# Kernel tuning notes

Hardware: AMD Instinct MI355X
Metric: run time of the kernel (lower is better)

Reference implementation:

```python
import jax, jax.numpy as jnp
import numpy as np

G, N, C, H, L = 128, 512, 64, 4, 4   # graphs, nodes/graph, channels, heads, layers
NT = G * N                            # 65536 total nodes
PE, IN_DIM, PROT = 16, 64, 128
DEG = 16
E = NT * DEG
EPS = 1e-5


def setup_inputs() -> dict:
    key = jax.random.key(0)
    ks = jax.random.split(key, 48)
    def w(k, shape):
        fan = shape[-2] if len(shape) >= 2 else shape[-1]
        return (jax.random.normal(k, shape, jnp.float32) / np.sqrt(fan)).astype(jnp.float32)
    inp = {}
    inp['x'] = jax.random.normal(ks[0], (NT, IN_DIM), jnp.float32)
    inp['pe'] = jax.random.normal(ks[1], (NT, PE), jnp.float32)
    inp['edge_index'] = jax.random.randint(ks[2], (2, E), 0, NT, dtype=jnp.int32)
    # embedding layers
    inp['node_emb_w'] = w(ks[3], (IN_DIM, C - PE)); inp['node_emb_b'] = jnp.zeros((C - PE,), jnp.float32)
    inp['pe_lin_w'] = w(ks[4], (PE, PE));           inp['pe_lin_b'] = jnp.zeros((PE,), jnp.float32)
    inp['pe_norm_g'] = jnp.ones((PE,), jnp.float32); inp['pe_norm_b'] = jnp.zeros((PE,), jnp.float32)
    # per-layer stacked params [L, ...]
    inp['gin_w1'] = w(ks[5], (L, C, C)); inp['gin_b1'] = jnp.zeros((L, C), jnp.float32)
    inp['gin_w2'] = w(ks[6], (L, C, C)); inp['gin_b2'] = jnp.zeros((L, C), jnp.float32)
    inp['attn_wq'] = w(ks[7], (L, C, C)); inp['attn_bq'] = jnp.zeros((L, C), jnp.float32)
    inp['attn_wk'] = w(ks[8], (L, C, C)); inp['attn_bk'] = jnp.zeros((L, C), jnp.float32)
    inp['attn_wv'] = w(ks[9], (L, C, C)); inp['attn_bv'] = jnp.zeros((L, C), jnp.float32)
    inp['attn_wo'] = w(ks[10], (L, C, C)); inp['attn_bo'] = jnp.zeros((L, C), jnp.float32)
    for i, nm in enumerate(['norm1', 'norm2', 'norm3']):
        inp[nm + '_g'] = jnp.ones((L, C), jnp.float32)
        inp[nm + '_b'] = jnp.zeros((L, C), jnp.float32)
    inp['mlp_w1'] = w(ks[11], (L, C, 2 * C)); inp['mlp_b1'] = jnp.zeros((L, 2 * C), jnp.float32)
    inp['mlp_w2'] = w(ks[12], (L, 2 * C, C)); inp['mlp_b2'] = jnp.zeros((L, C), jnp.float32)
    inp['head_w'] = w(ks[13], (C, PROT)); inp['head_b'] = jnp.zeros((PROT,), jnp.float32)
    return inp


def _bn(x, g, b):
    # BatchNorm1d, training-mode batch statistics (biased variance)
    mu = x.mean(axis=0)
    var = jnp.mean((x - mu) ** 2, axis=0)
    return (x - mu) * jax.lax.rsqrt(var + EPS) * g + b


def _mha(xd, wq, bq, wk, bk, wv, bv, wo, bo):
    # xd: [G, N, C] dense per-graph batch (all graphs equal size -> full mask)
    dh = C // H
    q = (xd @ wq + bq).reshape(G, N, H, dh)
    k = (xd @ wk + bk).reshape(G, N, H, dh)
    v = (xd @ wv + bv).reshape(G, N, H, dh)
    s = jnp.einsum('gqhd,gkhd->ghqk', q, k) * (1.0 / np.sqrt(dh))
    a = jax.nn.softmax(s, axis=-1)
    o = jnp.einsum('ghqk,gkhd->gqhd', a, v).reshape(G, N, C)
    return o @ wo + bo


def reference(x, pe, edge_index, node_emb_w, node_emb_b, pe_lin_w, pe_lin_b,
              pe_norm_g, pe_norm_b, gin_w1, gin_b1, gin_w2, gin_b2,
              attn_wq, attn_bq, attn_wk, attn_bk, attn_wv, attn_bv, attn_wo, attn_bo,
              norm1_g, norm1_b, norm2_g, norm2_b, norm3_g, norm3_b,
              mlp_w1, mlp_b1, mlp_w2, mlp_b2, head_w, head_b):
    src, dst = edge_index[0], edge_index[1]
    pe_n = _bn(pe, pe_norm_g, pe_norm_b)
    h = jnp.concatenate([x @ node_emb_w + node_emb_b, pe_n @ pe_lin_w + pe_lin_b], axis=1)  # [NT, C]
    for l in range(L):
        # local: GINConv (eps=0): nn(x + sum_j x_j) via gather + segment_sum
        agg = jax.ops.segment_sum(h[src], dst, num_segments=NT)
        z = h + agg
        hl = jax.nn.relu(z @ gin_w1[l] + gin_b1[l]) @ gin_w2[l] + gin_b2[l]
        hl = _bn(hl + h, norm1_g[l], norm1_b[l])
        # global: dense multihead self-attention per graph
        ha = _mha(h.reshape(G, N, C), attn_wq[l], attn_bq[l], attn_wk[l], attn_bk[l],
                  attn_wv[l], attn_bv[l], attn_wo[l], attn_bo[l]).reshape(NT, C)
        ha = _bn(ha + h, norm2_g[l], norm2_b[l])
        out = hl + ha
        out = out + (jax.nn.relu(out @ mlp_w1[l] + mlp_b1[l]) @ mlp_w2[l] + mlp_b2[l])
        h = _bn(out, norm3_g[l], norm3_b[l])
    pooled = h.reshape(G, N, C).mean(axis=1)  # global_mean_pool over equal-size graphs
    return pooled @ head_w + head_b
```

## Files before the change

### kernel.cpp

```cpp
#include <hip/hip_runtime.h>

typedef unsigned short ushort;
typedef unsigned int uint;
typedef __attribute__((ext_vector_type(8))) short short8;
typedef __attribute__((ext_vector_type(4))) float floatx4;

#define NTOT   65536
#define CH     64
#define NLAYER 4
#define NEDGE  1048576
#define EPSV   1e-5f

#define OW_EMB 0
#define OB_EMB 3072
#define OW_PE  3120
#define OB_PE  3376
#define OG_PEN 3392
#define OB_PEN 3408
#define OW_G1  3424
#define OB_G1  19808
#define OW_G2  20064
#define OB_G2  36448
#define OW_Q   36704
#define OB_Q   53088
#define OW_K   53344
#define OB_K   69728
#define OW_V   69984
#define OB_V   86368
#define OW_O   86624
#define OB_O   103008
#define ON1G   103264
#define ON1B   103520
#define ON2G   103776
#define ON2B   104032
#define ON3G   104288
#define ON3B   104544
#define OW_M1  104800
#define OB_M1  137568
#define OW_M2  138080
#define OB_M2  170848
#define OW_H   171104
#define OB_H   179296
#define TOTW   179424

__device__ __forceinline__ float bf2f(ushort u){ return __uint_as_float(((uint)u) << 16); }
__device__ __forceinline__ ushort f2bf(float f){
    uint u = __float_as_uint(f);
    uint r = (u + 0x7fffu + ((u >> 16) & 1u)) >> 16;
    return (ushort)r;
}
__device__ __forceinline__ float2 bfp2(uint w){
    return make_float2(__uint_as_float(w << 16), __uint_as_float(w & 0xffff0000u));
}
__device__ __forceinline__ short8 ldf(const ushort* p){ return *(const short8*)p; }
__device__ __forceinline__ floatx4 mfma16(short8 a, short8 b, floatx4 c){
    return __builtin_amdgcn_mfma_f32_16x16x32_bf16(a, b, c, 0, 0, 0);
}
__device__ __forceinline__ void bnfin(float* sf, const float* st, const ushort* g,
                                      const ushort* b, int ident, int t){
    if (t < 64){
        float a, bb;
        if (ident){ a = 1.f; bb = 0.f; }
        else {
            float mu  = st[t] * (1.f / NTOT);
            float var = st[64 + t] * (1.f / NTOT) - mu * mu;
            a = rsqrtf(var + EPSV) * bf2f(g[t]);
            bb = bf2f(b[t]) - mu * a;
        }
        sf[t] = a; sf[64 + t] = bb;
    }
}

__global__ void detect_k(const uint* __restrict__ x, int* __restrict__ flag){
    int lane = threadIdx.x;
    uint w = x[lane];
    uint e = (w >> 7) & 0xffu;
    int ok = (e >= 100u && e <= 140u) ? 1 : 0;
    unsigned long long m = __ballot(ok);
    if (lane == 0) flag[0] = (__popcll(m) >= 48) ? 1 : 0;
}

struct WPtrs { const void* p[30]; };

__global__ void convall_k(WPtrs ptrs, ushort* __restrict__ dst, const int* __restrict__ flag){
    const int offs[31] = {0,3072,3120,3376,3392,3408,3424,19808,20064,36448,36704,
                          53088,53344,69728,69984,86368,86624,103008,103264,103520,
                          103776,104032,104288,104544,104800,137568,138080,170848,
                          171104,179296,179424};
    const int kdt[30] = {64,0,16,0,0,0, 64,0,64,0, 64,0,64,0,64,0,64,0,
                         0,0,0,0,0,0, 64,0,128,0, 64,0};
    const int ndt[30] = {48,0,16,0,0,0, 64,0,64,0, 64,0,64,0,64,0,64,0,
                         0,0,0,0,0,0, 128,0,64,0, 128,0};
    int i = blockIdx.x * blockDim.x + threadIdx.x;
    if (i >= TOTW) return;
    int s = 0;
    while (s < 29 && i >= offs[s + 1]) ++s;
    int j = i - offs[s];
    int srcj = j;
    int K = kdt[s];
    if (K > 0){
        int N = ndt[s], KN = K * N;
        int l = j / KN, r = j - l * KN;
        int n = r / K, k2 = r - n * K;
        srcj = l * KN + k2 * N + n;
    }
    if (*flag) dst[i] = ((const ushort*)ptrs.p[s])[srcj];
    else       dst[i] = f2bf(((const float*)ptrs.p[s])[srcj]);
}

__global__ void pe_stats_k(const void* __restrict__ peraw, const int* __restrict__ flag,
                           float* __restrict__ stats){
    int bf = *flag;
    int t = threadIdx.x;
    int c = t & 15, rb = t >> 4;
    int row0 = blockIdx.x * 256;
    float s = 0.f, ss = 0.f;
    for (int i = 0; i < 16; ++i){
        int r = row0 + rb + 16 * i;
        size_t idx = (size_t)r * 16 + c;
        float v = bf ? bf2f(((const ushort*)peraw)[idx]) : ((const float*)peraw)[idx];
        s += v; ss += v * v;
    }
    __shared__ float red[256];
    red[t] = s; __syncthreads();
    if (t < 16){ float tot = 0.f; for (int j = 0; j < 16; ++j) tot += red[t + 16 * j]; atomicAdd(&stats[t], tot); }
    __syncthreads();
    red[t] = ss; __syncthreads();
    if (t < 16){ float tot = 0.f; for (int j = 0; j < 16; ++j) tot += red[t + 16 * j]; atomicAdd(&stats[64 + t], tot); }
}

__global__ void fin_k(const float* __restrict__ stats, const ushort* __restrict__ g,
                      const ushort* __restrict__ b, float* __restrict__ fin, int nch){
    int c = threadIdx.x;
    if (c >= nch) return;
    float mu  = stats[c] * (1.f / NTOT);
    float var = stats[64 + c] * (1.f / NTOT) - mu * mu;
    float a = rsqrtf(var + EPSV) * bf2f(g[c]);
    fin[c] = a;
    fin[64 + c] = bf2f(b[c]) - mu * a;
}

__global__ void embed_k(const void* __restrict__ xraw, const void* __restrict__ peraw,
                        const int* __restrict__ flag, const ushort* __restrict__ wsa,
                        const float* __restrict__ finpe, ushort* __restrict__ hout){
    __shared__ __align__(16) ushort xb[64 * 72];
    __shared__ __align__(16) ushort pen[64 * 24];
    __shared__ __align__(16) ushort Wes[48 * 72];
    __shared__ __align__(16) ushort Wps[16 * 24];
    int bf = *flag;
    int t = threadIdx.x;
    int row0 = blockIdx.x * 64;
    if (bf){
        const uint* xsrc = (const uint*)((const ushort*)xraw + (size_t)row0 * 64);
        for (int i = t; i < 2048; i += 256){
            int r = i >> 5, u = i & 31;
            ((uint*)(xb + r * 72))[u] = xsrc[i];
        }
    } else {
        const float4* xsrc = (const float4*)((const float*)xraw + (size_t)row0 * 64);
        for (int i = t; i < 1024; i += 256){
            int r = i >> 4, u = i & 15;
            float4 f = xsrc[i];
            ((uint*)(xb + r * 72))[2 * u]     = (uint)f2bf(f.x) | ((uint)f2bf(f.y) << 16);
            ((uint*)(xb + r * 72))[2 * u + 1] = (uint)f2bf(f.z) | ((uint)f2bf(f.w) << 16);
        }
    }
    for (int i = t; i < 1024; i += 256){
        int r = i >> 4, k = i & 15;
        size_t idx = (size_t)(row0 + r) * 16 + k;
        float v = bf ? bf2f(((const ushort*)peraw)[idx]) : ((const float*)peraw)[idx];
        pen[r * 24 + k] = f2bf(v * finpe[k] + finpe[64 + k]);
    }
    for (int i = t; i < 1536; i += 256){
        int r = i >> 5, u = i & 31;
        ((uint*)(Wes + r * 72))[u] = ((const uint*)(wsa + OW_EMB))[i];
    }
    {
        int r = t >> 4, k = t & 15;
        Wps[r * 24 + k] = wsa[OW_PE + t];
    }
    __syncthreads();
    int w = t >> 6, l = t & 63, m = l & 15, quad = l >> 4;
    const short8 zero8 = {0, 0, 0, 0, 0, 0, 0, 0};
    const floatx4 zf4 = {0.f, 0.f, 0.f, 0.f};
    const ushort* ap = xb + (16 * w + m) * 72 + quad * 8;
    short8 a0 = ldf(ap), a1 = ldf(ap + 32);
    short8 ape = (quad < 2) ? ldf(pen + (16 * w + m) * 24 + quad * 8) : zero8;
    #pragma unroll
    for (int nt = 0; nt < 4; ++nt){
        floatx4 c = zf4;
        float bias;
        if (nt < 3){
            const ushort* bp = Wes + (nt * 16 + m) * 72 + quad * 8;
            c = mfma16(a0, ldf(bp), c);
            c = mfma16(a1, ldf(bp + 32), c);
            bias = bf2f(wsa[OB_EMB + nt * 16 + m]);
        } else {
            short8 bpe = (quad < 2) ? ldf(Wps + m * 24 + quad * 8) : zero8;
            c = mfma16(ape, bpe, c);
            bias = bf2f(wsa[OB_PE + m]);
        }
        #pragma unroll
        for (int r = 0; r < 4; ++r)
            hout[(size_t)(row0 + 16 * w + quad * 4 + r) * 64 + nt * 16 + m] = f2bf(c[r] + bias);
    }
}

__global__ void hist_k(const int* __restrict__ dst, int* __restrict__ cnt){
    int stride = gridDim.x * blockDim.x;
    for (int e = blockIdx.x * blockDim.x + threadIdx.x; e < NEDGE; e += stride)
        atomicAdd(&cnt[dst[e]], 1);
}

__global__ void scan_k(const int* __restrict__ cnt, int* __restrict__ offs, int* __restrict__ cur){
    int t = threadIdx.x;
    int base0 = t * 64;
    int s = 0;
    for (int i = 0; i < 64; ++i) s += cnt[base0 + i];
    __shared__ int pref[1024];
    pref[t] = s; __syncthreads();
    for (int off = 1; off < 1024; off <<= 1){
        int v = (t >= off) ? pref[t - off] : 0;
        __syncthreads();
        pref[t] += v;
        __syncthreads();
    }
    int run = pref[t] - s;
    for (int i = 0; i < 64; ++i){
        offs[base0 + i] = run;
        cur[base0 + i]  = run;
        run += cnt[base0 + i];
    }
    if (t == 1023) offs[65536] = run;
}

__global__ void scatter_k(const int* __restrict__ src, const int* __restrict__ dst,
                          int* __restrict__ cur, int* __restrict__ csr){
    int stride = gridDim.x * blockDim.x;
    for (int e = blockIdx.x * blockDim.x + threadIdx.x; e < NEDGE; e += stride){
        int p = atomicAdd(&cur[dst[e]], 1);
        atomicExch(&csr[p], src[e]);
    }
}

__global__ void agg_k(const ushort* __restrict__ h, const int* __restrict__ offs,
                      const int* __restrict__ csr, ushort* __restrict__ z,
                      const float* __restrict__ st, const ushort* __restrict__ g,
                      const ushort* __restrict__ b, int ident){
    __shared__ float sf[128];
    int t = threadIdx.x;
    bnfin(sf, st, g, b, ident, t);
    __syncthreads();
    int w = t >> 6, l = t & 63;
    int node = blockIdx.x * 8 + w * 2 + (l >> 5);
    int c2 = l & 31;
    const uint* hp = (const uint*)h;
    int beg = offs[node], end = offs[node + 1];
    float2 s = bfp2(hp[(size_t)node * 32 + c2]);
    for (int i = beg; i < end; ++i){
        int sn = csr[i];
        float2 p = bfp2(hp[(size_t)sn * 32 + c2]);
        s.x += p.x; s.y += p.y;
    }
    float n = (float)(1 + end - beg);
    int c0 = c2 * 2;
    float o0 = sf[c0] * s.x + n * sf[64 + c0];
    float o1 = sf[c0 + 1] * s.y + n * sf[64 + c0 + 1];
    ((uint*)z)[(size_t)node * 32 + c2] = (uint)f2bf(o0) | ((uint)f2bf(o1) << 16);
}

__global__ void ginqkv_k(const ushort* __restrict__ z, const ushort* __restrict__ h,
                         const float* __restrict__ st3, const ushort* __restrict__ g3,
                         const ushort* __restrict__ b3, int ident,
                         const ushort* __restrict__ W1, const ushort* __restrict__ b1,
                         const ushort* __restrict__ W2, const ushort* __restrict__ b2,
                         const ushort* __restrict__ Wq, const ushort* __restrict__ bq,
                         const ushort* __restrict__ Wk, const ushort* __restrict__ bk,
                         const ushort* __restrict__ Wv, const ushort* __restrict__ bv,
                         ushort* __restrict__ zout, ushort* __restrict__ qo,
                         ushort* __restrict__ ko, ushort* __restrict__ vo,
                         float* __restrict__ stats){
    __shared__ __align__(16) ushort As[64 * 72];
    __shared__ __align__(16) ushort Hs[64 * 72];
    __shared__ __align__(16) ushort W1s[64 * 72];
    __shared__ __align__(16) ushort W2s[64 * 72];
    __shared__ __align__(16) ushort Wqs[64 * 72];
    __shared__ __align__(16) ushort Wks[64 * 72];
    __shared__ __align__(16) ushort Wvs[64 * 72];
    __shared__ float sb[128];
    __shared__ float sf[128];
    int t = threadIdx.x;
    int row0 = blockIdx.x * 64;
    bnfin(sf, st3, g3, b3, ident, t);
    if (t < 128) sb[t] = 0.f;
    __syncthreads();
    for (int i = t; i < 2048; i += 256){
        int r = i >> 5, u = i & 31;
        ((uint*)(As  + r * 72))[u] = ((const uint*)(z + (size_t)row0 * 64))[i];
        uint hv = ((const uint*)(h + (size_t)row0 * 64))[i];
        int c0 = u * 2;
        float2 p = bfp2(hv);
        ((uint*)(Hs + r * 72))[u] = (uint)f2bf(p.x * sf[c0] + sf[64 + c0])
                                  | ((uint)f2bf(p.y * sf[c0 + 1] + sf[64 + c0 + 1]) << 16);
        ((uint*)(W1s + r * 72))[u] = ((const uint*)W1)[i];
        ((uint*)(W2s + r * 72))[u] = ((const uint*)W2)[i];
        ((uint*)(Wqs + r * 72))[u] = ((const uint*)Wq)[i];
        ((uint*)(Wks + r * 72))[u] = ((const uint*)Wk)[i];
        ((uint*)(Wvs + r * 72))[u] = ((const uint*)Wv)[i];
    }
    __syncthreads();
    int w = t >> 6, l = t & 63, m = l & 15, q4 = l >> 4;
    const ushort* ap = As + (16 * w + m) * 72 + q4 * 8;
    short8 a0 = ldf(ap), a1 = ldf(ap + 32);
    const ushort* hpp = Hs + (16 * w + m) * 72 + q4 * 8;
    short8 h0 = ldf(hpp), h1 = ldf(hpp + 32);
    floatx4 acc[4];
    #pragma unroll
    for (int nt = 0; nt < 4; ++nt){
        const ushort* bp = W1s + (nt * 16 + m) * 72 + q4 * 8;
        floatx4 c = {0.f, 0.f, 0.f, 0.f};
        c = mfma16(a0, ldf(bp), c);
        c = mfma16(a1, ldf(bp + 32), c);
        acc[nt] = c;
    }
    #pragma unroll
    for (int nt = 0; nt < 4; ++nt){
        float bv = bf2f(b1[nt * 16 + m]);
        #pragma unroll
        for (int r = 0; r < 4; ++r)
            As[(16 * w + q4 * 4 + r) * 72 + nt * 16 + m] = f2bf(fmaxf(acc[nt][r] + bv, 0.f));
    }
    const ushort* ap2 = As + (16 * w + m) * 72 + q4 * 8;
    short8 t0 = ldf(ap2), t1 = ldf(ap2 + 32);
    #pragma unroll
    for (int nt = 0; nt < 4; ++nt){
        const ushort* bp = W2s + (nt * 16 + m) * 72 + q4 * 8;
        floatx4 c = {0.f, 0.f, 0.f, 0.f};
        c = mfma16(t0, ldf(bp), c);
        c = mfma16(t1, ldf(bp + 32), c);
        float bv = bf2f(b2[nt * 16 + m]);
        float vs = 0.f, vss = 0.f;
        #pragma unroll
        for (int r = 0; r < 4; ++r){
            int lr = 16 * w + q4 * 4 + r;
            float val = c[r] + bv + bf2f(Hs[lr * 72 + nt * 16 + m]);
            zout[(size_t)(row0 + lr) * 64 + nt * 16 + m] = f2bf(val);
            vs += val; vss += val * val;
        }
        vs  += __shfl_xor(vs, 16, 64);  vs  += __shfl_xor(vs, 32, 64);
        vss += __shfl_xor(vss, 16, 64); vss += __shfl_xor(vss, 32, 64);
        if (q4 == 0){
            atomicAdd(&sb[nt * 16 + m], vs);
            atomicAdd(&sb[64 + nt * 16 + m], vss);
        }
    }
    ushort* outs[3] = {qo, ko, vo};
    const ushort* bias[3] = {bq, bk, bv};
    const ushort* wmats[3] = {Wqs, Wks, Wvs};
    #pragma unroll
    for (int o = 0; o < 3; ++o){
        #pragma unroll
        for (int nt = 0; nt < 4; ++nt){
            const ushort* bp = wmats[o] + (nt * 16 + m) * 72 + q4 * 8;
            floatx4 c = {0.f, 0.f, 0.f, 0.f};
            c = mfma16(h0, ldf(bp), c);
            c = mfma16(h1, ldf(bp + 32), c);
            float bv2 = bf2f(bias[o][nt * 16 + m]);
            #pragma unroll
            for (int r = 0; r < 4; ++r)
                outs[o][(size_t)(row0 + 16 * w + q4 * 4 + r) * 64 + nt * 16 + m] = f2bf(c[r] + bv2);
        }
    }
    __syncthreads();
    if (t < 64){
        atomicAdd(&stats[t], sb[t]);
        atomicAdd(&stats[64 + t], sb[64 + t]);
    }
}

__global__ void attn_k(ushort* __restrict__ q, const ushort* __restrict__ k,
                       const ushort* __restrict__ v){
    __shared__ __align__(16) ushort Ks[512 * 24];
    __shared__ __align__(16) ushort Vt[16 * 536];
    int t = threadIdx.x;
    int g = blockIdx.x >> 2, head = blockIdx.x & 3;
    int base = g * 512;
    for (int i = t; i < 4096; i += 256){
        int n = i >> 3, u = i & 7;
        uint kw = ((const uint*)(k + (size_t)(base + n) * 64 + head * 16))[u];
        uint vw = ((const uint*)(v + (size_t)(base + n) * 64 + head * 16))[u];
        float2 kf = bfp2(kw);
        Ks[n * 24 + 2 * u]     = f2bf(kf.x * 0.25f);
        Ks[n * 24 + 2 * u + 1] = f2bf(kf.y * 0.25f);
        Vt[(2 * u) * 536 + n]     = (ushort)(vw & 0xffffu);
        Vt[(2 * u + 1) * 536 + n] = (ushort)(vw >> 16);
    }
    __syncthreads();
    int w = t >> 6, l = t & 63, m16 = l & 15, quad = l >> 4;
    const short8 zero8 = {0, 0, 0, 0, 0, 0, 0, 0};
    const floatx4 zf4 = {0.f, 0.f, 0.f, 0.f};
    int key1 = ((m16 >> 2) << 3) + (m16 & 3);

    for (int qi = 0; qi < 8; ++qi){
        int qt = w * 8 + qi;
        int qrow = base + qt * 16 + m16;
        short8 qf = zero8;
        if (quad < 2) qf = ldf(q + (size_t)qrow * 64 + head * 16 + quad * 8);
        floatx4 O = zf4;
        float mm = -1e30f, ll = 0.f;
        for (int kg = 0; kg < 16; ++kg){
            int kb = kg * 32;
            short8 af1 = zero8, af2 = zero8;
            if (quad < 2){
                const ushort* kp = Ks + (kb + key1) * 24 + quad * 8;
                af1 = ldf(kp);
                af2 = ldf(kp + 96);
            }
            floatx4 s1 = mfma16(af1, qf, zf4);
            floatx4 s2 = mfma16(af2, qf, zf4);
            float tm = fmaxf(fmaxf(fmaxf(s1[0], s1[1]), fmaxf(s1[2], s1[3])),
                             fmaxf(fmaxf(s2[0], s2[1]), fmaxf(s2[2], s2[3])));
            tm = fmaxf(tm, __shfl_xor(tm, 16, 64));
            tm = fmaxf(tm, __shfl_xor(tm, 32, 64));
            float mn = fmaxf(mm, tm);
            float c = __expf(mm - mn);
            float p0 = __expf(s1[0] - mn), p1 = __expf(s1[1] - mn);
            float p2 = __expf(s1[2] - mn), p3 = __expf(s1[3] - mn);
            float p4 = __expf(s2[0] - mn), p5 = __expf(s2[1] - mn);
            float p6 = __expf(s2[2] - mn), p7 = __expf(s2[3] - mn);
            float ts = ((p0 + p1) + (p2 + p3)) + ((p4 + p5) + (p6 + p7));
            ts += __shfl_xor(ts, 16, 64);
            ts += __shfl_xor(ts, 32, 64);
            ll = ll * c + ts;
            mm = mn;
            short8 pf;
            pf[0] = (short)f2bf(p0); pf[1] = (short)f2bf(p1);
            pf[2] = (short)f2bf(p2); pf[3] = (short)f2bf(p3);
            pf[4] = (short)f2bf(p4); pf[5] = (short)f2bf(p5);
            pf[6] = (short)f2bf(p6); pf[7] = (short)f2bf(p7);
            short8 vf = ldf(Vt + m16 * 536 + kb + quad * 8);
            O[0] *= c; O[1] *= c; O[2] *= c; O[3] *= c;
            O = mfma16(vf, pf, O);
        }
        float inv = 1.f / ll;
        uint lo = (uint)f2bf(O[0] * inv) | ((uint)f2bf(O[1] * inv) << 16);
        uint hi = (uint)f2bf(O[2] * inv) | ((uint)f2bf(O[3] * inv) << 16);
        uint2 st = {lo, hi};
        *(uint2*)(q + (size_t)qrow * 64 + head * 16 + quad * 4) = st;
    }
}

__global__ void oproj_k(ushort* __restrict__ o, const ushort* __restrict__ h,
                        const float* __restrict__ st3, const ushort* __restrict__ g3,
                        const ushort* __restrict__ b3, int ident,
                        const ushort* __restrict__ Wo, const ushort* __restrict__ bo,
                        float* __restrict__ stats){
    __shared__ __align__(16) ushort As[64 * 72];
    __shared__ __align__(16) ushort Ws[64 * 72];
    __shared__ float sb[128];
    __shared__ float sf[128];
    int t = threadIdx.x;
    int row0 = blockIdx.x * 64;
    bnfin(sf, st3, g3, b3, ident, t);
    if (t < 128) sb[t] = 0.f;
    __syncthreads();
    for (int i = t; i < 2048; i += 256){
        int r = i >> 5, u = i & 31;
        ((uint*)(As + r * 72))[u] = ((const uint*)(o + (size_t)row0 * 64))[i];
        ((uint*)(Ws + r * 72))[u] = ((const uint*)Wo)[i];
    }
    __syncthreads();
    int w = t >> 6, l = t & 63, m = l & 15, q4 = l >> 4;
    const ushort* ap = As + (16 * w + m) * 72 + q4 * 8;
    short8 a0 = ldf(ap), a1 = ldf(ap + 32);
    #pragma unroll
    for (int nt = 0; nt < 4; ++nt){
        const ushort* bp = Ws + (nt * 16 + m) * 72 + q4 * 8;
        floatx4 c = {0.f, 0.f, 0.f, 0.f};
        c = mfma16(a0, ldf(bp), c);
        c = mfma16(a1, ldf(bp + 32), c);
        int ch = nt * 16 + m;
        float bv = bf2f(bo[ch]);
        float ba = sf[ch], bb = sf[64 + ch];
        float vs = 0.f, vss = 0.f;
        #pragma unroll
        for (int r = 0; r < 4; ++r){
            size_t gi = (size_t)(row0 + 16 * w + q4 * 4 + r) * 64 + ch;
            float val = c[r] + bv + ba * bf2f(h[gi]) + bb;
            o[gi] = f2bf(val);
            vs += val; vss += val * val;
        }
        vs  += __shfl_xor(vs, 16, 64);  vs  += __shfl_xor(vs, 32, 64);
        vss += __shfl_xor(vss, 16, 64); vss += __shfl_xor(vss, 32, 64);
        if (q4 == 0){
            atomicAdd(&sb[ch], vs);
            atomicAdd(&sb[64 + ch], vss);
        }
    }
    __syncthreads();
    if (t < 64){
        atomicAdd(&stats[t], sb[t]);
        atomicAdd(&stats[64 + t], sb[64 + t]);
    }
}

__global__ void comb_k(const ushort* __restrict__ hlpre, const ushort* __restrict__ hapre,
                       const float* __restrict__ st1, const ushort* __restrict__ n1g,
                       const ushort* __restrict__ n1b,
                       const float* __restrict__ st2, const ushort* __restrict__ n2g,
                       const ushort* __restrict__ n2b,
                       const ushort* __restrict__ W1, const ushort* __restrict__ b1,
                       const ushort* __restrict__ W2, const ushort* __restrict__ b2,
                       ushort* __restrict__ hout, float* __restrict__ stats){
    __shared__ __align__(16) ushort Ob[64 * 72];
    __shared__ float Of[64 * 64];
    __shared__ __align__(16) ushort W1s[128 * 72];
    __shared__ __align__(16) ushort Hs[64 * 136];
    __shared__ __align__(16) ushort W2s[64 * 136];
    __shared__ float sb[128];
    __shared__ float sf1[128], sf2[128];
    int t = threadIdx.x;
    int row0 = blockIdx.x * 64;
    if (t < 128){
        const float* st = (t < 64) ? st1 : st2;
        const ushort* g = (t < 64) ? n1g : n2g;
        const ushort* b = (t < 64) ? n1b : n2b;
        float* f = (t < 64) ? sf1 : sf2;
        int c = t & 63;
        float mu  = st[c] * (1.f / NTOT);
        float var = st[64 + c] * (1.f / NTOT) - mu * mu;
        float a = rsqrtf(var + EPSV) * bf2f(g[c]);
        f[c] = a;
        f[64 + c] = bf2f(b[c]) - mu * a;
        sb[t] = 0.f;
    }
    __syncthreads();
    for (int i = t; i < 2048; i += 256){
        int r = i >> 5, u = i & 31;
        size_t gi = (size_t)(row0 + r) * 32 + u;
        uint wl = ((const uint*)hlpre)[gi], wa = ((const uint*)hapre)[gi];
        int c0 = u * 2;
        float2 pl = bfp2(wl), pa = bfp2(wa);
        float v0 = pl.x * sf1[c0] + sf1[64 + c0] + pa.x * sf2[c0] + sf2[64 + c0];
        float v1 = pl.y * sf1[c0 + 1] + sf1[64 + c0 + 1] + pa.y * sf2[c0 + 1] + sf2[64 + c0 + 1];
        ((uint*)(Ob + r * 72))[u] = (uint)f2bf(v0) | ((uint)f2bf(v1) << 16);
        Of[r * 64 + c0] = v0; Of[r * 64 + c0 + 1] = v1;
    }
    for (int i = t; i < 4096; i += 256){
        int r = i >> 5, u = i & 31;
        ((uint*)(W1s + r * 72))[u] = ((const uint*)W1)[i];
        int r2 = i >> 6, u2 = i & 63;
        ((uint*)(W2s + r2 * 136))[u2] = ((const uint*)W2)[i];
    }
    __syncthreads();
    int w = t >> 6, l = t & 63, m = l & 15, q4 = l >> 4;
    const ushort* ap = Ob + (16 * w + m) * 72 + q4 * 8;
    short8 a0 = ldf(ap), a1 = ldf(ap + 32);
    #pragma unroll
    for (int nt = 0; nt < 8; ++nt){
        const ushort* bp = W1s + (nt * 16 + m) * 72 + q4 * 8;
        floatx4 c = {0.f, 0.f, 0.f, 0.f};
        c = mfma16(a0, ldf(bp), c);
        c = mfma16(a1, ldf(bp + 32), c);
        float bv = bf2f(b1[nt * 16 + m]);
        #pragma unroll
        for (int r = 0; r < 4; ++r)
            Hs[(16 * w + q4 * 4 + r) * 136 + nt * 16 + m] = f2bf(fmaxf(c[r] + bv, 0.f));
    }
    const ushort* ap2 = Hs + (16 * w + m) * 136 + q4 * 8;
    short8 h0 = ldf(ap2), h1 = ldf(ap2 + 32), h2 = ldf(ap2 + 64), h3 = ldf(ap2 + 96);
    #pragma unroll
    for (int nt = 0; nt < 4; ++nt){
        const ushort* bp = W2s + (nt * 16 + m) * 136 + q4 * 8;
        floatx4 c = {0.f, 0.f, 0.f, 0.f};
        c = mfma16(h0, ldf(bp), c);
        c = mfma16(h1, ldf(bp + 32), c);
        c = mfma16(h2, ldf(bp + 64), c);
        c = mfma16(h3, ldf(bp + 96), c);
        float bv = bf2f(b2[nt * 16 + m]);
        float vs = 0.f, vss = 0.f;
        #pragma unroll
        for (int r = 0; r < 4; ++r){
            int lr = 16 * w + q4 * 4 + r;
            float val = c[r] + bv + Of[lr * 64 + nt * 16 + m];
            hout[(size_t)(row0 + lr) * 64 + nt * 16 + m] = f2bf(val);
            vs += val; vss += val * val;
        }
        vs  += __shfl_xor(vs, 16, 64);  vs  += __shfl_xor(vs, 32, 64);
        vss += __shfl_xor(vss, 16, 64); vss += __shfl_xor(vss, 32, 64);
        if (q4 == 0){
            atomicAdd(&sb[nt * 16 + m], vs);
            atomicAdd(&sb[64 + nt * 16 + m], vss);
        }
    }
    __syncthreads();
    if (t < 64){
        atomicAdd(&stats[t], sb[t]);
        atomicAdd(&stats[64 + t], sb[64 + t]);
    }
}

__global__ void pool_head_k(const ushort* __restrict__ h, const float* __restrict__ st3,
                            const ushort* __restrict__ g3, const ushort* __restrict__ b3,
                            const ushort* __restrict__ Wh, const ushort* __restrict__ bh,
                            const int* __restrict__ flag, void* __restrict__ out){
    __shared__ float red[256];
    __shared__ float pooled[64];
    __shared__ float sf[128];
    int t = threadIdx.x, g = blockIdx.x;
    bnfin(sf, st3, g3, b3, 0, t);
    int c = t & 63, rb = t >> 6;
    float s = 0.f;
    for (int ii = 0; ii < 128; ++ii){
        int r = rb + 4 * ii;
        s += bf2f(h[(size_t)(g * 512 + r) * 64 + c]);
    }
    red[t] = s; __syncthreads();
    if (t < 64)
        pooled[t] = sf[t] * ((red[t] + red[64 + t] + red[128 + t] + red[192 + t]) * (1.f / 512.f))
                  + sf[64 + t];
    __syncthreads();
    if (t < 128){
        float a = bf2f(bh[t]);
        #pragma unroll
        for (int k = 0; k < 64; ++k) a += pooled[k] * bf2f(Wh[t * 64 + k]);
        if (*flag) ((ushort*)out)[(size_t)g * 128 + t] = f2bf(a);
        else       ((float*)out)[(size_t)g * 128 + t] = a;
    }
}

extern "C" void kernel_launch(void* const* d_in, const int* in_sizes, int n_in,
                              void* d_out, int out_size, void* d_ws, size_t ws_size,
                              hipStream_t stream){
    const void* x  = d_in[0];
    const void* pe = d_in[1];
    const int* eidx = (const int*)d_in[2];

    char* ws = (char*)d_ws;
    const size_t MB = 1024 * 1024;
    const size_t KB = 1024;
    ushort* h_buf = (ushort*)(ws);
    ushort* z_buf = (ushort*)(ws + 8 * MB);
    ushort* q_buf = (ushort*)(ws + 16 * MB);
    ushort* k_buf = (ushort*)(ws + 24 * MB);
    ushort* v_buf = (ushort*)(ws + 32 * MB);
    int* csr   = (int*)(ws + 40 * MB);
    int* offs  = (int*)(ws + 44 * MB);
    int* cnt   = (int*)(ws + 44 * MB + 384 * KB);
    int* cur   = (int*)(ws + 44 * MB + 640 * KB);
    float* stats = (float*)(ws + 44 * MB + 896 * KB);
    float* fin   = (float*)(ws + 44 * MB + 904 * KB);
    int*   flag  = (int*)(ws + 44 * MB + 912 * KB);
    ushort* wsa  = (ushort*)(ws + 45 * MB);

    hipMemsetAsync(stats, 0, 13 * 128 * sizeof(float), stream);
    hipMemsetAsync(cnt, 0, 65536 * sizeof(int), stream);

    detect_k<<<1, 64, 0, stream>>>((const uint*)x, flag);

    WPtrs wp;
    for (int i = 0; i < 30; ++i) wp.p[i] = d_in[3 + i];
    convall_k<<<(TOTW + 255) / 256, 256, 0, stream>>>(wp, wsa, flag);

    pe_stats_k<<<256, 256, 0, stream>>>(pe, flag, stats);
    fin_k<<<1, 64, 0, stream>>>(stats, wsa + OG_PEN, wsa + OB_PEN, fin, 16);
    embed_k<<<1024, 256, 0, stream>>>(x, pe, flag, wsa, fin, h_buf);
    hist_k<<<1024, 256, 0, stream>>>(eidx + NEDGE, cnt);
    scan_k<<<1, 1024, 0, stream>>>(cnt, offs, cur);
    scatter_k<<<1024, 256, 0, stream>>>(eidx, eidx + NEDGE, cur, csr);

    for (int l = 0; l < NLAYER; ++l){
        float* st1 = stats + (1 + 3 * l) * 128;
        float* st2 = stats + (2 + 3 * l) * 128;
        float* st3 = stats + (3 + 3 * l) * 128;
        int ident = (l == 0) ? 1 : 0;
        const float* stp = (l == 0) ? stats : stats + (3 * l) * 128;
        const ushort* gp = wsa + ON3G + (l ? (l - 1) : 0) * 64;
        const ushort* bp = wsa + ON3B + (l ? (l - 1) : 0) * 64;

        agg_k<<<8192, 256, 0, stream>>>(h_buf, offs, csr, z_buf, stp, gp, bp, ident);
        ginqkv_k<<<1024, 256, 0, stream>>>(z_buf, h_buf, stp, gp, bp, ident,
                                           wsa + OW_G1 + l * 4096, wsa + OB_G1 + l * 64,
                                           wsa + OW_G2 + l * 4096, wsa + OB_G2 + l * 64,
                                           wsa + OW_Q + l * 4096, wsa + OB_Q + l * 64,
                                           wsa + OW_K + l * 4096, wsa + OB_K + l * 64,
                                           wsa + OW_V + l * 4096, wsa + OB_V + l * 64,
                                           z_buf, q_buf, k_buf, v_buf, st1);
        attn_k<<<512, 256, 0, stream>>>(q_buf, k_buf, v_buf);
        oproj_k<<<1024, 256, 0, stream>>>(q_buf, h_buf, stp, gp, bp, ident,
                                          wsa + OW_O + l * 4096, wsa + OB_O + l * 64, st2);
        comb_k<<<1024, 256, 0, stream>>>(z_buf, q_buf,
                                         st1, wsa + ON1G + l * 64, wsa + ON1B + l * 64,
                                         st2, wsa + ON2G + l * 64, wsa + ON2B + l * 64,
                                         wsa + OW_M1 + l * 8192, wsa + OB_M1 + l * 128,
                                         wsa + OW_M2 + l * 8192, wsa + OB_M2 + l * 64,
                                         h_buf, st3);
    }
    pool_head_k<<<128, 256, 0, stream>>>(h_buf, stats + 12 * 128,
                                         wsa + ON3G + 3 * 64, wsa + ON3B + 3 * 64,
                                         wsa + OW_H, wsa + OB_H, flag, d_out);
}
```

Measured before the change: 1.249 ms.

## Build CSR with two-pass shared-memory bucket sort and 16-bit indices

Replaces the per-edge global atomicAdd/atomicExch scatter with a two-pass build. Pass A bins edges into 256 destination buckets in LDS and writes them out in coalesced chunks with per-bucket global cursors. Pass B sorts each bucket by local node in LDS and writes a compact ushort CSR. Storing source indices as 16-bit also halves the CSR bytes the aggregation kernel reads in every layer. The risk is that it relies on a 65536-node limit and fixed LDS capacities (8192 edges per bucket), which skewed degree distributions could overflow.

```diff
diff --git a/kernel.cpp b/kernel.cpp
--- a/kernel.cpp
+++ b/kernel.cpp
@@ -10,6 +10,8 @@
 #define NLAYER 4
 #define NEDGE  1048576
 #define EPSV   1e-5f
+#define NBKT   256
+#define BCAP   48
 
 #define OW_EMB 0
 #define OB_EMB 3072
@@ -212,7 +214,8 @@
         atomicAdd(&cnt[dst[e]], 1);
 }
 
-__global__ void scan_k(const int* __restrict__ cnt, int* __restrict__ offs, int* __restrict__ cur){
+__global__ void scan_k(const int* __restrict__ cnt, int* __restrict__ offs,
+                       int* __restrict__ bcur){
     int t = threadIdx.x;
     int base0 = t * 64;
     int s = 0;
@@ -227,24 +230,68 @@
     }
     int run = pref[t] - s;
     for (int i = 0; i < 64; ++i){
-        offs[base0 + i] = run;
-        cur[base0 + i]  = run;
-        run += cnt[base0 + i];
+        int node = base0 + i;
+        offs[node] = run;
+        if ((node & 255) == 0) bcur[node >> 8] = run;
+        run += cnt[node];
     }
     if (t == 1023) offs[65536] = run;
 }
 
-__global__ void scatter_k(const int* __restrict__ src, const int* __restrict__ dst,
-                          int* __restrict__ cur, int* __restrict__ csr){
-    int stride = gridDim.x * blockDim.x;
-    for (int e = blockIdx.x * blockDim.x + threadIdx.x; e < NEDGE; e += stride){
-        int p = atomicAdd(&cur[dst[e]], 1);
-        atomicExch(&csr[p], src[e]);
-    }
+__global__ __launch_bounds__(256) void passA_k(const int* __restrict__ src,
+                                               const int* __restrict__ dst,
+                                               int* __restrict__ bcur,
+                                               uint* __restrict__ stage){
+    __shared__ uint bins[NBKT * BCAP];
+    __shared__ int bcnt[NBKT];
+    int t = threadIdx.x;
+    bcnt[t] = 0;
+    __syncthreads();
+    int e0 = blockIdx.x * 4096;
+    for (int i = t; i < 4096; i += 256){
+        int e = e0 + i;
+        int sv = src[e], dv = dst[e];
+        int b = dv >> 8;
+        uint packed = ((uint)sv << 16) | (uint)(dv & 255);
+        int pos = atomicAdd(&bcnt[b], 1);
+        if (pos < BCAP) bins[b * BCAP + pos] = packed;
+        else { int gp = atomicAdd(&bcur[b], 1); stage[gp] = packed; }
+    }
+    __syncthreads();
+    int w = t >> 6, l = t & 63;
+    for (int b = w; b < NBKT; b += 4){
+        int c = bcnt[b]; if (c > BCAP) c = BCAP;
+        int pos = 0;
+        if (l == 0 && c > 0) pos = atomicAdd(&bcur[b], c);
+        pos = __shfl(pos, 0, 64);
+        if (l < c) stage[pos + l] = bins[b * BCAP + l];
+    }
+}
+
+__global__ __launch_bounds__(256) void passB_k(const uint* __restrict__ stage,
+                                               const int* __restrict__ offs,
+                                               ushort* __restrict__ csr){
+    __shared__ ushort lcsr[8192];
+    __shared__ int lcur[256];
+    int t = threadIdx.x;
+    int nbeg = blockIdx.x * 256;
+    int base = offs[nbeg];
+    int size = offs[nbeg + 256] - base;
+    lcur[t] = offs[nbeg + t] - base;
+    __syncthreads();
+    for (int i = t; i < size; i += 256){
+        uint e = stage[base + i];
+        int nl = e & 255;
+        int lp = atomicAdd(&lcur[nl], 1);
+        lcsr[lp] = (ushort)(e >> 16);
+    }
+    __syncthreads();
+    for (int i = t; i < size; i += 256)
+        csr[base + i] = lcsr[i];
 }
 
 __global__ void agg_k(const ushort* __restrict__ h, const int* __restrict__ offs,
-                      const int* __restrict__ csr, ushort* __restrict__ z,
+                      const ushort* __restrict__ csr, ushort* __restrict__ z,
                       const float* __restrict__ st, const ushort* __restrict__ g,
                       const ushort* __restrict__ b, int ident){
     __shared__ float sf[128];
@@ -644,14 +691,15 @@
     ushort* q_buf = (ushort*)(ws + 16 * MB);
     ushort* k_buf = (ushort*)(ws + 24 * MB);
     ushort* v_buf = (ushort*)(ws + 32 * MB);
-    int* csr   = (int*)(ws + 40 * MB);
-    int* offs  = (int*)(ws + 44 * MB);
-    int* cnt   = (int*)(ws + 44 * MB + 384 * KB);
-    int* cur   = (int*)(ws + 44 * MB + 640 * KB);
-    float* stats = (float*)(ws + 44 * MB + 896 * KB);
-    float* fin   = (float*)(ws + 44 * MB + 904 * KB);
-    int*   flag  = (int*)(ws + 44 * MB + 912 * KB);
-    ushort* wsa  = (ushort*)(ws + 45 * MB);
+    uint*   stage = (uint*)(ws + 40 * MB);
+    ushort* csr   = (ushort*)(ws + 44 * MB);
+    int* offs  = (int*)(ws + 46 * MB);
+    int* cnt   = (int*)(ws + 46 * MB + 320 * KB);
+    int* bcur  = (int*)(ws + 46 * MB + 640 * KB);
+    float* stats = (float*)(ws + 47 * MB);
+    float* fin   = (float*)(ws + 47 * MB + 8 * KB);
+    int*   flag  = (int*)(ws + 47 * MB + 16 * KB);
+    ushort* wsa  = (ushort*)(ws + 47 * MB + 20 * KB);
 
     hipMemsetAsync(stats, 0, 13 * 128 * sizeof(float), stream);
     hipMemsetAsync(cnt, 0, 65536 * sizeof(int), stream);
@@ -666,8 +714,9 @@
     fin_k<<<1, 64, 0, stream>>>(stats, wsa + OG_PEN, wsa + OB_PEN, fin, 16);
     embed_k<<<1024, 256, 0, stream>>>(x, pe, flag, wsa, fin, h_buf);
     hist_k<<<1024, 256, 0, stream>>>(eidx + NEDGE, cnt);
-    scan_k<<<1, 1024, 0, stream>>>(cnt, offs, cur);
-    scatter_k<<<1024, 256, 0, stream>>>(eidx, eidx + NEDGE, cur, csr);
+    scan_k<<<1, 1024, 0, stream>>>(cnt, offs, bcur);
+    passA_k<<<256, 256, 0, stream>>>(eidx, eidx + NEDGE, bcur, stage);
+    passB_k<<<256, 256, 0, stream>>>(stage, offs, csr);
 
     for (int l = 0; l < NLAYER; ++l){
         float* st1 = stats + (1 + 3 * l) * 128;
```

Result: slower. 1.474 ms (+18.0%).
